# Kernel tuning notes

Measured on AMD Instinct MI355X. Metric: run time of the kernel, lower is better.

Reference implementation:

```python
import jax, jax.numpy as jnp
import numpy as np

K_SIZE = 12      # patch kernel/stride (non-overlapping)
H, W_IMG = 60, 108
PH, PW = H // K_SIZE, W_IMG // K_SIZE
L = PH * PW
N_LAYERS = 133
EPS = 1e-12


def _unfold(x):
    # x: [B, C, 60, 108] -> [B, C*12*12, 45], matching torch.nn.Unfold ordering
    B, C = x.shape[0], x.shape[1]
    x = x.reshape(B, C, PH, K_SIZE, PW, K_SIZE)          # (b,c,ph,ki,pw,kj)
    x = x.transpose(0, 1, 3, 5, 2, 4)                    # (b,c,ki,kj,ph,pw)
    return x.reshape(B, C * K_SIZE * K_SIZE, L)


def _fold(y, C=3):
    # y: [B, C*144, 45] -> [B, C, 60, 108] (non-overlapping, so fold = inverse reshape)
    B = y.shape[0]
    y = y.reshape(B, C, K_SIZE, K_SIZE, PH, PW)          # (b,c,ki,kj,ph,pw)
    y = y.transpose(0, 1, 4, 2, 5, 3)                    # (b,c,ph,ki,pw,kj)
    return y.reshape(B, C, H, W_IMG)


def setup_inputs() -> dict:
    key = jax.random.key(0)
    k1, k2, k3 = jax.random.split(key, 3)
    I = jax.random.normal(k1, (4, 3, H, W_IMG), dtype=jnp.float32)
    S = jax.random.uniform(k2, (4, H, W_IMG, N_LAYERS), dtype=jnp.float32)
    M = jax.random.uniform(k3, (4, 1, H, W_IMG), dtype=jnp.float32)
    return {"I": I, "S": S, "M": M}


def reference(I, S, M):
    bt = I.shape[0]
    Iu = I[..., None]                  # [bt,3,60,108,1]
    Se = S[:, None]                    # [bt,1,60,108,N]
    Me = M[..., None]                  # [bt,1,60,108,1]
    U = Iu * Se * Me                   # [bt,3,60,108,N]
    Kt = Iu * Se * (1.0 - Me)
    # permute(0,4,1,2,3).reshape(bt*N, 3, 60, 108)
    U = U.transpose(0, 4, 1, 2, 3).reshape(bt * N_LAYERS, 3, H, W_IMG)
    Kt = Kt.transpose(0, 4, 1, 2, 3).reshape(bt * N_LAYERS, 3, H, W_IMG)
    Ku = _unfold(Kt)                   # [B, 432, 45]
    Uu = _unfold(U)                    # [B, 432, 45]
    # affinity: bmm(U^T, K) -> [B, 45, 45]
    Wm = jnp.einsum('bcp,bcq->bpq', Uu, Ku)
    # F.normalize(p=1, dim=-1): divide by max(L1 norm, eps)
    l1 = jnp.maximum(jnp.sum(jnp.abs(Wm), axis=-1, keepdims=True), EPS)
    Wm = Wm / l1
    # weighted sum: WK[b,c,i] = sum_j W[b,i,j] * K[b,c,j]  (same math as the
    # original broadcast multiply+sum, expressed as a batched matmul)
    WK = jnp.einsum('bij,bcj->bci', Wm, Ku)              # [B, 432, 45]
    out = _fold(WK)                                       # [B, 3, 60, 108]
    out = out.reshape(bt, N_LAYERS, 3, H, W_IMG).sum(axis=1)
    return I * (1.0 - M) + out * M
```

## Files before the change

kernel.cpp:

```cpp
#include <hip/hip_runtime.h>

#define NL 133
#define HT 60
#define WD 108
#define PIX (HT*WD)
#define CT 432
#define L45 45
#define STR 440
#define BTC 4
#define NB (BTC*NL)
#define EPIX (3*PIX)

typedef _Float16 f16;
typedef _Float16 h4v __attribute__((ext_vector_type(4)));
typedef _Float16 h8v __attribute__((ext_vector_type(8)));
typedef float f32x4 __attribute__((ext_vector_type(4)));

__device__ __forceinline__ f32x4 mfma_k32(h8v a, h8v b, f32x4 c){
  return __builtin_amdgcn_mfma_f32_16x16x32_f16(a, b, c, 0, 0, 0);
}
__device__ __forceinline__ f32x4 mfma_k16(h4v a, h4v b, f32x4 c){
  return __builtin_amdgcn_mfma_f32_16x16x16f16(a, b, c, 0, 0, 0);
}

__global__ __launch_bounds__(256) void kprep(const float* __restrict__ S,
                                             const float* __restrict__ I,
                                             const float* __restrict__ M,
                                             f16* __restrict__ Su,
                                             f16* __restrict__ IMu,
                                             f16* __restrict__ IKu){
  __shared__ float tile[64][135];
  int blk = blockIdx.x;
  int tid = threadIdx.x;
  if (blk < BTC*102){
    int bt = blk / 102, t = blk % 102;
    int pix0 = t * 64;
    for (int r = tid; r < 64*NL; r += 256){
      int p = r / NL, nn = r % NL;
      int pix = pix0 + p;
      if (pix < PIX) tile[p][nn] = S[((size_t)bt*PIX + pix)*NL + nn];
    }
    __syncthreads();
    for (int w = tid; w < 64*NL; w += 256){
      int nn = w / 64, pp = w % 64;
      int pix = pix0 + pp;
      if (pix < PIX){
        int y = pix / WD, x = pix % WD;
        int py = y/12, ky = y%12, px = x/12, kx = x%12;
        int pa = py*9 + px, kr = ky*12 + kx;
        Su[(size_t)(bt*NL + nn)*PIX + pa*144 + kr] = (f16)tile[pp][nn];
      }
    }
  } else {
    int b2 = blk - BTC*102;
    int bt = b2 / L45, pa = b2 % L45;
    int py = pa/9, px = pa%9;
    const float* Ib = I + (size_t)bt*EPIX;
    const float* Mb = M + (size_t)bt*PIX;
    for (int c = tid; c < CT; c += 256){
      int ch = c/144, kr = c%144;
      int ky = kr/12, kx = kr%12;
      int pix = (py*12 + ky)*WD + px*12 + kx;
      float iv = Ib[ch*PIX + pix];
      float mv = Mb[pix];
      IMu[((size_t)bt*L45 + pa)*CT + c] = (f16)(iv*mv);
      IKu[((size_t)bt*L45 + pa)*CT + c] = (f16)(iv*(1.f - mv));
    }
  }
}

template<bool USE_SCR>
__global__ __launch_bounds__(256) void kmain(const f16* __restrict__ IMu,
                                             const f16* __restrict__ IKu,
                                             const f16* __restrict__ Su,
                                             f16* __restrict__ scr,
                                             float* __restrict__ outAcc){
  __shared__ f16 lds[(L45 + 48)*STR];
  f16* bufU = lds;
  f16* bufK = lds + L45*STR;

  int b  = blockIdx.x;
  int bt = b / NL;
  int tid = threadIdx.x;

  for (int z = tid; z < 3*STR; z += 256) bufK[L45*STR + z] = (f16)0.f;

  {
    const f16* IMb = IMu + (size_t)bt*L45*CT;
    const f16* IKb = IKu + (size_t)bt*L45*CT;
    const f16* Sb  = Su  + (size_t)b*PIX;
    for (int slot = tid; slot < L45*54; slot += 256){
      int p = slot / 54, cg = slot % 54;
      int c0 = cg*8;
      h8v im = *(const h8v*)&IMb[p*CT + c0];
      h8v ik = *(const h8v*)&IKb[p*CT + c0];
      h8v sv = *(const h8v*)&Sb[p*144 + (c0 % 144)];
      *(h8v*)&bufU[p*STR + c0] = im*sv;
      *(h8v*)&bufK[p*STR + c0] = ik*sv;
    }
  }
  __syncthreads();

  int wid  = tid >> 6;
  int lane = tid & 63;
  int lrow = lane & 15, lgrp = lane >> 4;

  f32x4 acc0 = {0.f,0.f,0.f,0.f}, acc1 = acc0, acc2 = acc0;
  int t0 = wid;
  int t1 = wid + 4;
  int t2 = (wid + 8 < 9) ? wid + 8 : 8;
  int ti0 = t0/3, tj0 = t0%3;
  int ti1 = t1/3, tj1 = t1%3;
  int ti2 = t2/3, tj2 = t2%3;

  const f16* uA0 = &bufU[(ti0*16 + lrow)*STR];
  const f16* uA1 = &bufU[(ti1*16 + lrow)*STR];
  const f16* uA2 = &bufU[(ti2*16 + lrow)*STR];
  const f16* kB0 = &bufK[(tj0*16 + lrow)*STR];
  const f16* kB1 = &bufK[(tj1*16 + lrow)*STR];
  const f16* kB2 = &bufK[(tj2*16 + lrow)*STR];

  for (int ks = 0; ks < 13; ++ks){
    int c0 = ks*32 + lgrp*8;
    h8v a0 = *(const h8v*)&uA0[c0];
    h8v a1 = *(const h8v*)&uA1[c0];
    h8v a2 = *(const h8v*)&uA2[c0];
    h8v b0 = *(const h8v*)&kB0[c0];
    h8v b1 = *(const h8v*)&kB1[c0];
    h8v b2 = *(const h8v*)&kB2[c0];
    acc0 = mfma_k32(a0, b0, acc0);
    acc1 = mfma_k32(a1, b1, acc1);
    acc2 = mfma_k32(a2, b2, acc2);
  }
  {
    int c0 = 416 + lgrp*4;
    h4v a0 = *(const h4v*)&uA0[c0];
    h4v a1 = *(const h4v*)&uA1[c0];
    h4v a2 = *(const h4v*)&uA2[c0];
    h4v b0 = *(const h4v*)&kB0[c0];
    h4v b1 = *(const h4v*)&kB1[c0];
    h4v b2 = *(const h4v*)&kB2[c0];
    acc0 = mfma_k16(a0, b0, acc0);
    acc1 = mfma_k16(a1, b1, acc1);
    acc2 = mfma_k16(a2, b2, acc2);
  }
  __syncthreads();

  float* Wm32 = (float*)lds;
  f16*   Wm16 = (f16*)((char*)lds + 48*49*4);
  {
    #pragma unroll
    for (int r = 0; r < 4; ++r){
      Wm32[(ti0*16 + lgrp*4 + r)*49 + tj0*16 + lrow] = acc0[r];
      Wm32[(ti1*16 + lgrp*4 + r)*49 + tj1*16 + lrow] = acc1[r];
      Wm32[(ti2*16 + lgrp*4 + r)*49 + tj2*16 + lrow] = acc2[r];
    }
  }
  __syncthreads();

  if (tid < L45){
    float rs = 0.f;
    for (int q = 0; q < L45; ++q) rs += fabsf(Wm32[tid*49 + q]);
    float inv = 1.0f / fmaxf(rs, 1e-12f);
    for (int j = 0; j < 48; ++j)
      Wm16[tid*48 + j] = (j < L45) ? (f16)(Wm32[tid*49 + j]*inv) : (f16)0.f;
  }
  __syncthreads();

  h8v aw0 = *(const h8v*)&Wm16[( 0 + lrow)*48 + lgrp*8];
  h8v aw1 = *(const h8v*)&Wm16[(16 + lrow)*48 + lgrp*8];
  h8v aw2 = *(const h8v*)&Wm16[(32 + lrow)*48 + lgrp*8];
  h4v at0 = *(const h4v*)&Wm16[( 0 + lrow)*48 + 32 + lgrp*4];
  h4v at1 = *(const h4v*)&Wm16[(16 + lrow)*48 + 32 + lgrp*4];
  h4v at2 = *(const h4v*)&Wm16[(32 + lrow)*48 + 32 + lgrp*4];

  for (int cb = wid; cb < 27; cb += 4){
    int cbase = cb*16 + lrow;
    h8v bK; h4v bT;
    #pragma unroll
    for (int r = 0; r < 8; ++r) bK[r] = bufK[(lgrp*8 + r)*STR + cbase];
    #pragma unroll
    for (int r = 0; r < 4; ++r) bT[r] = bufK[(32 + lgrp*4 + r)*STR + cbase];

    int ch  = cb / 9;
    int kr  = (cb % 9)*16 + lrow;
    int ky  = kr / 12, kx = kr - ky*12;
    int pixc = ch*PIX + ky*WD + kx;

    f32x4 d0 = {0.f,0.f,0.f,0.f}, d1 = d0, d2 = d0;
    d0 = mfma_k32(aw0, bK, d0);  d0 = mfma_k16(at0, bT, d0);
    d1 = mfma_k32(aw1, bK, d1);  d1 = mfma_k16(at1, bT, d1);
    d2 = mfma_k32(aw2, bK, d2);  d2 = mfma_k16(at2, bT, d2);

    #pragma unroll
    for (int r = 0; r < 4; ++r){
      { int i = 0 + lgrp*4 + r;
        int iy = i/9, ix = i - iy*9;
        int pix = pixc + (iy*12)*WD + ix*12;
        if (USE_SCR) scr[(size_t)b*EPIX + pix] = (f16)d0[r];
        else atomicAdd(&outAcc[(size_t)bt*EPIX + pix], (float)d0[r]); }
      { int i = 16 + lgrp*4 + r;
        int iy = i/9, ix = i - iy*9;
        int pix = pixc + (iy*12)*WD + ix*12;
        if (USE_SCR) scr[(size_t)b*EPIX + pix] = (f16)d1[r];
        else atomicAdd(&outAcc[(size_t)bt*EPIX + pix], (float)d1[r]); }
      { int i = 32 + lgrp*4 + r;
        if (i < L45){
          int iy = i/9, ix = i - iy*9;
          int pix = pixc + (iy*12)*WD + ix*12;
          if (USE_SCR) scr[(size_t)b*EPIX + pix] = (f16)d2[r];
          else atomicAdd(&outAcc[(size_t)bt*EPIX + pix], (float)d2[r]); } }
    }
  }
}

__global__ __launch_bounds__(256) void kreduce(const float* __restrict__ I,
                                               const float* __restrict__ M,
                                               const f16* __restrict__ scr,
                                               float* __restrict__ out){
  int t = blockIdx.x*256 + threadIdx.x;
  int sub = t & 7, g = t >> 3;
  if (g >= BTC*EPIX/4) return;
  int e4 = g*4;
  int bt = e4 / EPIX, e = e4 % EPIX;
  const f16* p = scr + (size_t)bt*NL*EPIX + e;
  float a0=0.f, a1=0.f, a2=0.f, a3=0.f;
  for (int nn = sub; nn < NL; nn += 8){
    h4v v = *(const h4v*)&p[(size_t)nn*EPIX];
    a0 += (float)v[0]; a1 += (float)v[1]; a2 += (float)v[2]; a3 += (float)v[3];
  }
  #pragma unroll
  for (int s = 1; s < 8; s <<= 1){
    a0 += __shfl_xor(a0, s); a1 += __shfl_xor(a1, s);
    a2 += __shfl_xor(a2, s); a3 += __shfl_xor(a3, s);
  }
  if (sub == 0){
    int pixb = e % PIX;
    const float* Mb = M + (size_t)bt*PIX;
    float4 iv = *(const float4*)&I[e4];
    float m0 = Mb[pixb], m1 = Mb[pixb+1], m2 = Mb[pixb+2], m3 = Mb[pixb+3];
    float4 o;
    o.x = iv.x*(1.f-m0) + a0*m0;
    o.y = iv.y*(1.f-m1) + a1*m1;
    o.z = iv.z*(1.f-m2) + a2*m2;
    o.w = iv.w*(1.f-m3) + a3*m3;
    *(float4*)&out[e4] = o;
  }
}

__global__ __launch_bounds__(256) void kfinal(const float* __restrict__ I,
                                              const float* __restrict__ M,
                                              float* __restrict__ out){
  int g = blockIdx.x*256 + threadIdx.x;
  if (g >= BTC*EPIX) return;
  int bt = g / EPIX, e = g % EPIX;
  float a = out[g];
  float m = M[bt*PIX + (e % PIX)];
  out[g] = I[g]*(1.f - m) + a*m;
}

extern "C" void kernel_launch(void* const* d_in, const int* in_sizes, int n_in,
                              void* d_out, int out_size, void* d_ws, size_t ws_size,
                              hipStream_t stream){
  const float* I = (const float*)d_in[0];
  const float* S = (const float*)d_in[1];
  const float* M = (const float*)d_in[2];
  float* out = (float*)d_out;

  const size_t needSu  = (size_t)NB*PIX*sizeof(f16);
  const size_t needIM  = (size_t)BTC*L45*CT*sizeof(f16);
  const size_t needScr = (size_t)NB*EPIX*sizeof(f16);
  const size_t prepSz  = needSu + 2*needIM;

  f16* Su  = (f16*)d_ws;
  f16* IMu = (f16*)((char*)d_ws + needSu);
  f16* IKu = (f16*)((char*)d_ws + needSu + needIM);
  f16* scr = (f16*)((char*)d_ws + prepSz);
  bool useScr = ws_size >= prepSz + needScr;

  kprep<<<BTC*102 + BTC*L45, 256, 0, stream>>>(S, I, M, Su, IMu, IKu);

  if (useScr){
    kmain<true ><<<NB, 256, 0, stream>>>(IMu, IKu, Su, scr, out);
    kreduce<<<((BTC*EPIX/4)*8 + 255)/256, 256, 0, stream>>>(I, M, scr, out);
  } else {
    (void)hipMemsetAsync(out, 0, (size_t)BTC*EPIX*sizeof(float), stream);
    kmain<false><<<NB, 256, 0, stream>>>(IMu, IKu, Su, scr, out);
    kfinal<<<(BTC*EPIX + 255)/256, 256, 0, stream>>>(I, M, out);
  }
}
```

Before: 113.8 us.

## Store scratch in patch-major unfolded layout and fold during reduction

The main kernel now writes its per-layer f16 results to scratch in the unfolded [patch][channel*144] layout, so lanes write contiguous channel indices instead of scattered image pixels. The reduction kernel reads that layout, sums over the 133 layers with a fully unrolled, clamped loop, and applies the fold index mapping only once when writing the final output. The goal is more coalesced scratch stores in the main kernel and fewer index computations, at the cost of more complex index math in the reduction and redundant clamped loads for the tail layers.

```diff
diff --git a/kernel.cpp b/kernel.cpp
--- a/kernel.cpp
+++ b/kernel.cpp
@@ -174,6 +174,7 @@
   h4v at1 = *(const h4v*)&Wm16[(16 + lrow)*48 + 32 + lgrp*4];
   h4v at2 = *(const h4v*)&Wm16[(32 + lrow)*48 + 32 + lgrp*4];
 
+  f16* sb = scr + (size_t)b*L45*CT;
   for (int cb = wid; cb < 27; cb += 4){
     int cbase = cb*16 + lrow;
     h8v bK; h4v bT;
@@ -195,21 +196,21 @@
     #pragma unroll
     for (int r = 0; r < 4; ++r){
       { int i = 0 + lgrp*4 + r;
-        int iy = i/9, ix = i - iy*9;
-        int pix = pixc + (iy*12)*WD + ix*12;
-        if (USE_SCR) scr[(size_t)b*EPIX + pix] = (f16)d0[r];
-        else atomicAdd(&outAcc[(size_t)bt*EPIX + pix], (float)d0[r]); }
+        if (USE_SCR) sb[(size_t)i*CT + cbase] = (f16)d0[r];
+        else {
+          int iy = i/9, ix = i - iy*9;
+          atomicAdd(&outAcc[(size_t)bt*EPIX + pixc + (iy*12)*WD + ix*12], (float)d0[r]); } }
       { int i = 16 + lgrp*4 + r;
-        int iy = i/9, ix = i - iy*9;
-        int pix = pixc + (iy*12)*WD + ix*12;
-        if (USE_SCR) scr[(size_t)b*EPIX + pix] = (f16)d1[r];
-        else atomicAdd(&outAcc[(size_t)bt*EPIX + pix], (float)d1[r]); }
+        if (USE_SCR) sb[(size_t)i*CT + cbase] = (f16)d1[r];
+        else {
+          int iy = i/9, ix = i - iy*9;
+          atomicAdd(&outAcc[(size_t)bt*EPIX + pixc + (iy*12)*WD + ix*12], (float)d1[r]); } }
       { int i = 32 + lgrp*4 + r;
         if (i < L45){
-          int iy = i/9, ix = i - iy*9;
-          int pix = pixc + (iy*12)*WD + ix*12;
-          if (USE_SCR) scr[(size_t)b*EPIX + pix] = (f16)d2[r];
-          else atomicAdd(&outAcc[(size_t)bt*EPIX + pix], (float)d2[r]); } }
+          if (USE_SCR) sb[(size_t)i*CT + cbase] = (f16)d2[r];
+          else {
+            int iy = i/9, ix = i - iy*9;
+            atomicAdd(&outAcc[(size_t)bt*EPIX + pixc + (iy*12)*WD + ix*12], (float)d2[r]); } } }
     }
   }
 }
@@ -220,31 +221,40 @@
                                                float* __restrict__ out){
   int t = blockIdx.x*256 + threadIdx.x;
   int sub = t & 7, g = t >> 3;
-  if (g >= BTC*EPIX/4) return;
-  int e4 = g*4;
-  int bt = e4 / EPIX, e = e4 % EPIX;
-  const f16* p = scr + (size_t)bt*NL*EPIX + e;
-  float a0=0.f, a1=0.f, a2=0.f, a3=0.f;
-  for (int nn = sub; nn < NL; nn += 8){
-    h4v v = *(const h4v*)&p[(size_t)nn*EPIX];
-    a0 += (float)v[0]; a1 += (float)v[1]; a2 += (float)v[2]; a3 += (float)v[3];
+  if (g >= BTC*L45*108) return;
+  int bt = g / (L45*108), rem = g % (L45*108);
+  int pa = rem / 108, c4 = rem % 108;
+  int c0 = c4*4;
+  const f16* p = scr + ((size_t)(bt*NL)*L45 + pa)*CT + c0;
+  f32x4 a = {0.f,0.f,0.f,0.f};
+  #pragma unroll
+  for (int k = 0; k < 17; ++k){
+    int nn = sub + k*8;
+    int nc = nn < NL ? nn : NL-1;
+    h4v v = *(const h4v*)&p[(size_t)nc*L45*CT];
+    if (nn < NL){
+      a[0] += (float)v[0]; a[1] += (float)v[1];
+      a[2] += (float)v[2]; a[3] += (float)v[3];
+    }
   }
   #pragma unroll
   for (int s = 1; s < 8; s <<= 1){
-    a0 += __shfl_xor(a0, s); a1 += __shfl_xor(a1, s);
-    a2 += __shfl_xor(a2, s); a3 += __shfl_xor(a3, s);
+    a[0] += __shfl_xor(a[0], s); a[1] += __shfl_xor(a[1], s);
+    a[2] += __shfl_xor(a[2], s); a[3] += __shfl_xor(a[3], s);
   }
   if (sub == 0){
-    int pixb = e % PIX;
-    const float* Mb = M + (size_t)bt*PIX;
-    float4 iv = *(const float4*)&I[e4];
-    float m0 = Mb[pixb], m1 = Mb[pixb+1], m2 = Mb[pixb+2], m3 = Mb[pixb+3];
+    int ch = c0/144, kr = c0%144, ky = kr/12, kx = kr%12;
+    int py = pa/9, px = pa%9;
+    int pix = (py*12 + ky)*WD + px*12 + kx;
+    size_t io = (size_t)bt*EPIX + ch*PIX + pix;
+    float4 iv = *(const float4*)&I[io];
+    float4 mv = *(const float4*)&M[(size_t)bt*PIX + pix];
     float4 o;
-    o.x = iv.x*(1.f-m0) + a0*m0;
-    o.y = iv.y*(1.f-m1) + a1*m1;
-    o.z = iv.z*(1.f-m2) + a2*m2;
-    o.w = iv.w*(1.f-m3) + a3*m3;
-    *(float4*)&out[e4] = o;
+    o.x = iv.x*(1.f-mv.x) + a[0]*mv.x;
+    o.y = iv.y*(1.f-mv.y) + a[1]*mv.y;
+    o.z = iv.z*(1.f-mv.z) + a[2]*mv.z;
+    o.w = iv.w*(1.f-mv.w) + a[3]*mv.w;
+    *(float4*)&out[io] = o;
   }
 }
 
@@ -269,7 +279,7 @@
 
   const size_t needSu  = (size_t)NB*PIX*sizeof(f16);
   const size_t needIM  = (size_t)BTC*L45*CT*sizeof(f16);
-  const size_t needScr = (size_t)NB*EPIX*sizeof(f16);
+  const size_t needScr = (size_t)NB*L45*CT*sizeof(f16);
   const size_t prepSz  = needSu + 2*needIM;
 
   f16* Su  = (f16*)d_ws;
@@ -282,7 +292,7 @@
 
   if (useScr){
     kmain<true ><<<NB, 256, 0, stream>>>(IMu, IKu, Su, scr, out);
-    kreduce<<<((BTC*EPIX/4)*8 + 255)/256, 256, 0, stream>>>(I, M, scr, out);
+    kreduce<<<((BTC*L45*108)*8 + 255)/256, 256, 0, stream>>>(I, M, scr, out);
   } else {
     (void)hipMemsetAsync(out, 0, (size_t)BTC*EPIX*sizeof(float), stream);
     kmain<false><<<NB, 256, 0, stream>>>(IMu, IKu, Su, scr, out);
```

Result: faster. 111.2 us (-2.3%).
